# Kernel tuning notes

Hardware: AMD Instinct MI355X
Metric: run time of the kernel (lower is better)

Reference implementation:

```python
import jax, jax.numpy as jnp
import numpy as np

B, C, D, H, W = 8, 256, 128, 64, 64  # batch, in_channels, inter_dim, spatial
BN_EPS = 1e-5


def setup_inputs() -> dict:
    key = jax.random.key(0)
    ks = jax.random.split(key, 6)
    s_c = 1.0 / np.sqrt(C)
    s_d = 1.0 / np.sqrt(D)
    return {
        "x": jax.random.normal(ks[0], (B, C, H, W), dtype=jnp.float32),
        # 1x1 conv kernels, stored as [out_ch, in_ch]
        "theta_w": jax.random.normal(ks[1], (D, C), dtype=jnp.float32) * s_c,
        "phi_w": jax.random.normal(ks[2], (D, C), dtype=jnp.float32) * s_c,
        "g_w": jax.random.normal(ks[3], (D, C), dtype=jnp.float32) * s_c,
        "w_w": jax.random.normal(ks[4], (C, D), dtype=jnp.float32) * s_d,
        "w_b": jnp.zeros((C,), dtype=jnp.float32),
        "bn_gamma": jnp.ones((C,), dtype=jnp.float32),
        "bn_beta": jnp.zeros((C,), dtype=jnp.float32),
    }


def reference(x, theta_w, phi_w, g_w, w_w, w_b, bn_gamma, bn_beta):
    Bs, Cs, Hs, Ws = x.shape
    N = Hs * Ws
    xf = x.reshape(Bs, Cs, N)  # flatten spatial -> [B, C, N]

    # 1x1 convs (bias=False) == per-position channel matmuls
    theta = jnp.einsum('dc,bcn->bnd', theta_w, xf)  # [B, N, D]
    phi = jnp.einsum('dc,bcn->bdn', phi_w, xf)      # [B, D, N]
    g = jnp.einsum('dc,bcn->bnd', g_w, xf)          # [B, N, D]

    # embedded-Gaussian attention: softmax(theta @ phi) @ g
    f = jnp.einsum('bnd,bdm->bnm', theta, phi)      # [B, N, N]
    f_div_C = jax.nn.softmax(f, axis=-1)
    y = jnp.einsum('bnm,bmd->bnd', f_div_C, g)      # [B, N, D]

    # output projection W (1x1 conv with bias)
    w_y = jnp.einsum('cd,bnd->bcn', w_w, y) + w_b[None, :, None]  # [B, C, N]

    # BatchNorm (training mode: batch statistics, biased variance)
    mean = w_y.mean(axis=(0, 2))
    var = jnp.mean(jnp.square(w_y - mean[None, :, None]), axis=(0, 2))
    scale = (bn_gamma * jax.lax.rsqrt(var + BN_EPS))[None, :, None]
    w_y = (w_y - mean[None, :, None]) * scale + bn_beta[None, :, None]

    z = w_y + xf  # residual
    return z.reshape(Bs, Cs, Hs, Ws)
```

## Files before the change

### kernel.cpp

```cpp
#include <hip/hip_runtime.h>

#define BB 8
#define CC 256
#define DD 128
#define NN 4096
#define BN_EPS 1e-5f
#define NSPLIT 4

typedef _Float16 f16;
typedef _Float16 half8 __attribute__((ext_vector_type(8)));
typedef _Float16 half2t __attribute__((ext_vector_type(2)));
typedef float f32x4 __attribute__((ext_vector_type(4)));

__device__ __forceinline__ f32x4 mfma16(half8 a, half8 b, f32x4 c) {
  return __builtin_amdgcn_mfma_f32_16x16x32_f16(a, b, c, 0, 0, 0);
}

__device__ __forceinline__ void gload_lds16(const void* g, void* l) {
  __builtin_amdgcn_global_load_lds((const __attribute__((address_space(1))) void*)g,
                                   (__attribute__((address_space(3))) void*)l, 16, 0, 0);
}

__device__ __forceinline__ half2t pkrtz(float a, float b) {
  auto t = __builtin_amdgcn_cvt_pkrtz(a, b);
  return __builtin_bit_cast(half2t, t);
}

#define EXP2(x) __builtin_amdgcn_exp2f(x)

#define PERM32(i) ((((i) >> 2) & 3) * 8 + (((i) >> 4) & 1) * 4 + ((i) & 3))

__global__ void k_cast_weights(const float* __restrict__ tw, const float* __restrict__ pw,
                               const float* __restrict__ gw, const float* __restrict__ ww,
                               f16* __restrict__ Wcat, f16* __restrict__ Wwh,
                               float* __restrict__ stats) {
  int i = blockIdx.x * 256 + threadIdx.x;
  if (i < 32768) Wcat[i] = (f16)tw[i];
  else if (i < 65536) Wcat[i] = (f16)pw[i - 32768];
  else if (i < 98304) Wcat[i] = (f16)gw[i - 65536];
  else if (i < 131072) Wwh[i - 98304] = (f16)ww[i - 98304];
  if (i < 512) stats[i] = 0.f;
}

__global__ __launch_bounds__(256) void k_gemm1(const float* __restrict__ x, const f16* __restrict__ Wcat,
                                               f16* __restrict__ T, f16* __restrict__ P,
                                               f16* __restrict__ Gdn) {
  __shared__ char xls[32768];
  __shared__ char gls[16384];
  int b = blockIdx.y;
  int n0 = blockIdx.x * 64;
  int tid = threadIdx.x;
  int lane = tid & 63, wave = tid >> 6;
  int lr = lane & 15, lg = lane >> 4;
  int wr = wave >> 1, wc = wave & 1;

  {
    int c = tid;
    const float* src = x + ((size_t)b * CC + c) * NN + n0;
#pragma unroll
    for (int n4 = 0; n4 < 64; n4 += 4) {
      f32x4 v = *(const f32x4*)(src + n4);
#pragma unroll
      for (int k = 0; k < 4; ++k) {
        int n = n4 + k;
        *(f16*)(xls + n * 512 + ((((c >> 3) ^ (n & 7)) * 8 + (c & 7)) * 2)) = (f16)v[k];
      }
    }
  }
  __syncthreads();

  half8 a[2][8];
#pragma unroll
  for (int i = 0; i < 2; ++i) {
    int nloc = wr * 32 + i * 16 + lr;
#pragma unroll
    for (int k0 = 0; k0 < 8; ++k0)
      a[i][k0] = *(const half8*)(xls + nloc * 512 + (((k0 * 4 + lg) ^ (nloc & 7)) << 4));
  }

  size_t base = (size_t)b * NN + n0;
#pragma unroll
  for (int yb = 0; yb < 6; ++yb) {
    int c0 = yb * 64 + wc * 32;
    f32x4 acc[2][2] = {};
#pragma unroll
    for (int k0 = 0; k0 < 8; ++k0) {
      half8 w[2];
      for (int j = 0; j < 2; ++j)
        w[j] = *(const half8*)(Wcat + (size_t)(c0 + j * 16 + lr) * CC + k0 * 32 + lg * 8);
      for (int i = 0; i < 2; ++i)
        for (int j = 0; j < 2; ++j)
          acc[i][j] = mfma16(a[i][k0], w[j], acc[i][j]);
    }
    if (yb < 4) {
      f16* dst = (yb < 2) ? T : P;
      int cl0 = (yb & 1) * 64 + wc * 32;
      for (int i = 0; i < 2; ++i)
        for (int j = 0; j < 2; ++j)
          for (int r = 0; r < 4; ++r) {
            int row = wr * 32 + i * 16 + lg * 4 + r;
            int col = cl0 + j * 16 + lr;
            dst[(base + row) * DD + col] = (f16)acc[i][j][r];
          }
    } else {
      for (int i = 0; i < 2; ++i)
        for (int j = 0; j < 2; ++j)
          for (int r = 0; r < 4; ++r) {
            int n = wr * 32 + i * 16 + lg * 4 + r;
            int d = (yb - 4) * 64 + wc * 32 + j * 16 + lr;
            *(f16*)(gls + n * 256 + ((((d >> 3) ^ (n & 7)) * 8 + (d & 7)) * 2)) = (f16)acc[i][j][r];
          }
    }
  }
  __syncthreads();
  {
    int d = tid >> 1, nh = (tid & 1) * 32;
    f16 tmp[32];
#pragma unroll
    for (int k = 0; k < 32; ++k) {
      int n = nh + k;
      tmp[k] = *(const f16*)(gls + n * 256 + ((((d >> 3) ^ (n & 7)) * 8 + (d & 7)) * 2));
    }
    f16* dst = Gdn + ((size_t)b * DD + d) * NN + n0 + nh;
#pragma unroll
    for (int k = 0; k < 4; ++k)
      *(half8*)(dst + k * 8) = *(const half8*)(tmp + k * 8);
  }
}

__global__ __launch_bounds__(256, 3) void k_flash(const f16* __restrict__ T, const f16* __restrict__ P,
                                                  const f16* __restrict__ Gdn, f16* __restrict__ accs,
                                                  float* __restrict__ ml) {
  __shared__ char smem[32768];
  int bid = blockIdx.x;
  int b = bid & 7;
  int u = bid >> 3;
  int hf = u & 3;
  int qx = u >> 2;
  int t0 = hf * 32;
  const int nt = 32;
  int tid = threadIdx.x;
  int lane = tid & 63, wave = tid >> 6;
  int lr = lane & 15, lg = lane >> 4;
  int q0 = qx * 128 + wave * 32;
  const f16* Tb = T + (size_t)b * NN * DD;
  const f16* Pb = P + ((size_t)b * NN + t0 * 32) * DD;
  const f16* Vb = Gdn + (size_t)b * DD * NN + t0 * 32;
  int srcq = 4 * lg;

  const f16* kbase[2];
  const f16* vbase[2];
  char* kdst[2];
  char* vdst[2];
#pragma unroll
  for (int inst = 0; inst < 2; ++inst) {
    int t = inst * 256 + tid;
    int row = t >> 4, sp = t & 15, sl = sp ^ (row & 7);
    kbase[inst] = Pb + (size_t)PERM32(row) * DD + sl * 8;
    kdst[inst] = smem + (inst * 256 + wave * 64) * 16;
    int dv = t >> 2, gv = t & 3, glv = gv ^ ((dv >> 1) & 3);
    vbase[inst] = Vb + (size_t)dv * NN + glv * 8;
    vdst[inst] = smem + 16384 + (inst * 256 + wave * 64) * 16;
  }

  half8 qf[2][4];
  for (int qt = 0; qt < 2; ++qt)
    for (int ks = 0; ks < 4; ++ks) {
      half8 v = *(const half8*)(Tb + (size_t)(q0 + qt * 16 + lr) * DD + ks * 32 + lg * 8);
      for (int j = 0; j < 8; ++j) v[j] *= (f16)1.44269504f;
      qf[qt][ks] = v;
    }
  half8 ones;
  for (int j = 0; j < 8; ++j) ones[j] = (f16)1.f;

  f32x4 acc[2][8] = {};
  f32x4 lsum[2] = {};
  float m_run[2] = {-1e30f, -1e30f};

#pragma unroll
  for (int inst = 0; inst < 2; ++inst) gload_lds16(kbase[inst], kdst[inst]);
#pragma unroll
  for (int inst = 0; inst < 2; ++inst) gload_lds16(vbase[inst], vdst[inst]);

  for (int kb = 0; kb < nt; ++kb) {
    int keyn = (kb < nt - 1) ? kb * 32 + 32 : 0;
    int cur = (kb & 1) * 8192, nxt = ((kb + 1) & 1) * 8192;
    char* Kc = smem + cur;
    char* Vc = smem + 16384 + cur;

    size_t ko = (size_t)keyn * DD;
#pragma unroll
    for (int inst = 0; inst < 2; ++inst) gload_lds16(kbase[inst] + ko, kdst[inst] + nxt);
    asm volatile("s_waitcnt vmcnt(4)" ::: "memory");
    __builtin_amdgcn_sched_barrier(0);
    __builtin_amdgcn_s_barrier();
    __builtin_amdgcn_sched_barrier(0);

    f32x4 s[2][2];
    __builtin_amdgcn_s_setprio(1);
    for (int kt = 0; kt < 2; ++kt) {
      half8 kf[4];
      for (int ks = 0; ks < 4; ++ks)
        kf[ks] = *(const half8*)(Kc + (kt * 16 + lr) * 256 + (((ks * 4 + lg) ^ (lr & 7)) << 4));
      for (int qt = 0; qt < 2; ++qt) {
        f32x4 t = {};
        for (int ks = 0; ks < 4; ++ks) t = mfma16(kf[ks], qf[qt][ks], t);
        s[qt][kt] = t;
      }
    }
    __builtin_amdgcn_s_setprio(0);

    half8 af[2];
    for (int qt = 0; qt < 2; ++qt) {
      float mx = fmaxf(fmaxf(s[qt][0][0], s[qt][0][1]), fmaxf(s[qt][0][2], s[qt][0][3]));
      mx = fmaxf(mx, fmaxf(fmaxf(s[qt][1][0], s[qt][1][1]), fmaxf(s[qt][1][2], s[qt][1][3])));
      mx = fmaxf(mx, __shfl_xor(mx, 16));
      mx = fmaxf(mx, __shfl_xor(mx, 32));
      bool grow = mx > m_run[qt] + 11.5f;
      if (__ballot(grow)) {
        float mn = fmaxf(m_run[qt], mx);
        float corr = EXP2(m_run[qt] - mn);
        m_run[qt] = mn;
        float c0 = __shfl(corr, srcq + 0), c1 = __shfl(corr, srcq + 1);
        float c2 = __shfl(corr, srcq + 2), c3 = __shfl(corr, srcq + 3);
        lsum[qt][0] *= c0; lsum[qt][1] *= c1; lsum[qt][2] *= c2; lsum[qt][3] *= c3;
        for (int nb = 0; nb < 8; ++nb) {
          acc[qt][nb][0] *= c0; acc[qt][nb][1] *= c1;
          acc[qt][nb][2] *= c2; acc[qt][nb][3] *= c3;
        }
      }
      for (int kt = 0; kt < 2; ++kt)
        for (int r = 0; r < 4; ++r)
          s[qt][kt][r] = EXP2(s[qt][kt][r] - m_run[qt]);
      union { half8 h8; half2t h2[4]; } un;
      un.h2[0] = pkrtz(s[qt][0][0], s[qt][0][1]);
      un.h2[1] = pkrtz(s[qt][0][2], s[qt][0][3]);
      un.h2[2] = pkrtz(s[qt][1][0], s[qt][1][1]);
      un.h2[3] = pkrtz(s[qt][1][2], s[qt][1][3]);
      af[qt] = un.h8;
      lsum[qt] = mfma16(af[qt], ones, lsum[qt]);
    }

#pragma unroll
    for (int inst = 0; inst < 2; ++inst) gload_lds16(vbase[inst] + keyn, vdst[inst] + nxt);
    asm volatile("s_waitcnt vmcnt(4)" ::: "memory");
    __builtin_amdgcn_sched_barrier(0);
    __builtin_amdgcn_s_barrier();
    __builtin_amdgcn_sched_barrier(0);

    __builtin_amdgcn_s_setprio(1);
    for (int nb = 0; nb < 8; ++nb) {
      int d = nb * 16 + lr;
      half8 vf = *(const half8*)(Vc + d * 64 + ((lg ^ ((d >> 1) & 3)) << 4));
      acc[0][nb] = mfma16(af[0], vf, acc[0][nb]);
      acc[1][nb] = mfma16(af[1], vf, acc[1][nb]);
    }
    __builtin_amdgcn_s_setprio(0);
  }
  asm volatile("s_waitcnt vmcnt(0)" ::: "memory");

  size_t gq0 = (size_t)b * NN + q0;
  f16* A = accs + (size_t)hf * ((size_t)BB * NN * DD) + gq0 * DD;
  for (int qt = 0; qt < 2; ++qt)
    for (int nb = 0; nb < 8; ++nb)
      for (int r = 0; r < 4; ++r)
        A[(size_t)(qt * 16 + lg * 4 + r) * DD + nb * 16 + lr] = (f16)acc[qt][nb][r];
  float* mArr = ml + hf * 32768;
  float* lArr = ml + NSPLIT * 32768 + hf * 32768;
  if (lg == 0) {
    mArr[gq0 + lr] = m_run[0];
    mArr[gq0 + 16 + lr] = m_run[1];
  }
  if (lr == 0)
    for (int r = 0; r < 4; ++r) {
      lArr[gq0 + lg * 4 + r] = lsum[0][r];
      lArr[gq0 + 16 + lg * 4 + r] = lsum[1][r];
    }
}

__global__ __launch_bounds__(256) void k_gemm2(const f16* __restrict__ Y, const float* __restrict__ ml,
                                               const f16* __restrict__ Wwh, const float* __restrict__ wb,
                                               f16* __restrict__ wy, float* __restrict__ stats) {
  __shared__ float part[2][8][256];
  const size_t SEG = (size_t)BB * NN * DD;
  int lane = threadIdx.x & 63, wave = threadIdx.x >> 6;
  int lr = lane & 15, lg = lane >> 4;
  int wr = wave >> 1, wc = wave & 1;
  float ps[4][2][2] = {};
  for (int mt = 0; mt < 2; ++mt) {
    int m0 = (blockIdx.x * 2 + mt) * 64 + wr * 32;
    f16 ch[2][NSPLIT];
    for (int i = 0; i < 2; ++i) {
      int row = m0 + i * 16 + lr;
      float m[NSPLIT], l[NSPLIT];
      float mm = -1e30f;
      for (int s = 0; s < NSPLIT; ++s) {
        m[s] = ml[s * 32768 + row];
        l[s] = ml[NSPLIT * 32768 + s * 32768 + row];
        mm = fmaxf(mm, m[s]);
      }
      float den = 0.f, c[NSPLIT];
      for (int s = 0; s < NSPLIT; ++s) {
        c[s] = EXP2(m[s] - mm);
        den += l[s] * c[s];
      }
      float inv = 1.f / den;
      for (int s = 0; s < NSPLIT; ++s) ch[i][s] = (f16)(c[s] * inv);
    }
    half8 a[2][4];
    for (int i = 0; i < 2; ++i)
      for (int k0 = 0; k0 < 4; ++k0) {
        size_t off = (size_t)(m0 + i * 16 + lr) * DD + k0 * 32 + lg * 8;
        half8 acc8 = *(const half8*)(Y + off) * ch[i][0];
        for (int s = 1; s < NSPLIT; ++s)
          acc8 = acc8 + *(const half8*)(Y + s * SEG + off) * ch[i][s];
        a[i][k0] = acc8;
      }
    for (int yb = 0; yb < 4; ++yb) {
      int c0 = yb * 64 + wc * 32;
      f32x4 acc[2][2] = {};
      for (int k0 = 0; k0 < 4; ++k0) {
        half8 w[2];
        for (int j = 0; j < 2; ++j)
          w[j] = *(const half8*)(Wwh + (size_t)(c0 + j * 16 + lr) * DD + k0 * 32 + lg * 8);
        for (int i = 0; i < 2; ++i)
          for (int j = 0; j < 2; ++j)
            acc[i][j] = mfma16(a[i][k0], w[j], acc[i][j]);
      }
      for (int i = 0; i < 2; ++i)
        for (int j = 0; j < 2; ++j) {
          float bias = wb[c0 + j * 16 + lr];
          for (int r = 0; r < 4; ++r) {
            int row = m0 + i * 16 + lg * 4 + r;
            int col = c0 + j * 16 + lr;
            float v = acc[i][j][r] + bias;
            wy[(size_t)row * CC + col] = (f16)v;
            ps[yb][j][0] += v;
            ps[yb][j][1] += v * v;
          }
        }
    }
  }
  for (int yb = 0; yb < 4; ++yb)
    for (int j = 0; j < 2; ++j) {
      int col = yb * 64 + wc * 32 + j * 16 + lr;
      part[0][wr * 4 + lg][col] = ps[yb][j][0];
      part[1][wr * 4 + lg][col] = ps[yb][j][1];
    }
  __syncthreads();
  {
    int col = threadIdx.x;
    for (int metric = 0; metric < 2; ++metric) {
      float s = 0.f;
      for (int wtr = 0; wtr < 8; ++wtr) s += part[metric][wtr][col];
      atomicAdd(&stats[metric * CC + col], s);
    }
  }
}

__global__ void k_bn_apply(const f16* __restrict__ wy, const float* __restrict__ x,
                           const float* __restrict__ stats, const float* __restrict__ gamma,
                           const float* __restrict__ beta, float* __restrict__ out) {
  __shared__ f16 tile[32][33];
  int b = blockIdx.z, c0 = blockIdx.y * 32, n0 = blockIdx.x * 32;
  int tx = threadIdx.x, ty = threadIdx.y;
  for (int j = 0; j < 4; ++j) {
    int nn = ty + j * 8;
    tile[nn][tx] = wy[((size_t)b * NN + n0 + nn) * CC + c0 + tx];
  }
  __syncthreads();
  const float inv_cnt = 1.f / (float)(BB * NN);
  for (int j = 0; j < 4; ++j) {
    int cc = ty + j * 8;
    int c = c0 + cc;
    float mean = stats[c] * inv_cnt;
    float var = stats[CC + c] * inv_cnt - mean * mean;
    float scale = gamma[c] * rsqrtf(var + BN_EPS);
    size_t oi = ((size_t)b * CC + c) * NN + n0 + tx;
    out[oi] = ((float)tile[tx][cc] - mean) * scale + beta[c] + x[oi];
  }
}

extern "C" void kernel_launch(void* const* d_in, const int* in_sizes, int n_in,
                              void* d_out, int out_size, void* d_ws, size_t ws_size,
                              hipStream_t stream) {
  const float* x = (const float*)d_in[0];
  const float* tw = (const float*)d_in[1];
  const float* pw = (const float*)d_in[2];
  const float* gw = (const float*)d_in[3];
  const float* ww = (const float*)d_in[4];
  const float* wb = (const float*)d_in[5];
  const float* gamma = (const float*)d_in[6];
  const float* beta = (const float*)d_in[7];
  float* out = (float*)d_out;
  char* ws = (char*)d_ws;

  f16* Wcat = (f16*)(ws + 0);
  f16* Wwh = (f16*)(ws + 196608);
  float* stats = (float*)(ws + 262144);
  float* ml = (float*)(ws + 524288);
  const size_t BASE = 1 << 21;
  f16* T = (f16*)(ws + BASE);
  f16* P = (f16*)(ws + BASE + 8388608);
  f16* Gdn = (f16*)(ws + BASE + 16777216);
  f16* accs = (f16*)(ws + BASE + 25165824);
  f16* wy = (f16*)(ws + BASE);

  k_cast_weights<<<512, 256, 0, stream>>>(tw, pw, gw, ww, Wcat, Wwh, stats);
  k_gemm1<<<dim3(NN / 64, BB), 256, 0, stream>>>(x, Wcat, T, P, Gdn);
  k_flash<<<1024, 256, 0, stream>>>(T, P, Gdn, accs, ml);
  k_gemm2<<<256, 256, 0, stream>>>(accs, ml, Wwh, wb, wy, stats);
  k_bn_apply<<<dim3(NN / 32, CC / 32, BB), dim3(32, 8), 0, stream>>>(wy, x, stats, gamma, beta, out);
}
```

Before: 167.3 us.

## Split flash KV range three ways and vectorize BN-apply transpose

Changes the flash-attention key/value split from four to three chunks (43/43/42 tiles of 32), reducing the grid from 1024 to 768 blocks so it better matches CU count and occupancy and cuts partial-result merge work. The BN-apply kernel is rewritten to process a 64-position by 256-channel tile per block with half8 loads and float4 loads/stores, replacing scalar 32x32 tiles. The uneven split and the gemm2 merge must agree on NSPLIT. The LDS transpose writes may cause bank conflicts.

New measurement: 161.3 us. 1.04x faster.

```diff
diff --git a/kernel.cpp b/kernel.cpp
--- a/kernel.cpp
+++ b/kernel.cpp
@@ -5,10 +5,11 @@
 #define DD 128
 #define NN 4096
 #define BN_EPS 1e-5f
-#define NSPLIT 4
+#define NSPLIT 3
 
 typedef _Float16 f16;
 typedef _Float16 half8 __attribute__((ext_vector_type(8)));
+typedef _Float16 half4 __attribute__((ext_vector_type(4)));
 typedef _Float16 half2t __attribute__((ext_vector_type(2)));
 typedef float f32x4 __attribute__((ext_vector_type(4)));
 
@@ -135,10 +136,10 @@
   int bid = blockIdx.x;
   int b = bid & 7;
   int u = bid >> 3;
-  int hf = u & 3;
-  int qx = u >> 2;
-  int t0 = hf * 32;
-  const int nt = 32;
+  int hf = u % 3;
+  int qx = u / 3;
+  int t0 = (hf == 2) ? 86 : hf * 43;
+  int nt = (hf == 2) ? 42 : 43;
   int tid = threadIdx.x;
   int lane = tid & 63, wave = tid >> 6;
   int lr = lane & 15, lg = lane >> 4;
@@ -358,26 +359,47 @@
   }
 }
 
-__global__ void k_bn_apply(const f16* __restrict__ wy, const float* __restrict__ x,
-                           const float* __restrict__ stats, const float* __restrict__ gamma,
-                           const float* __restrict__ beta, float* __restrict__ out) {
-  __shared__ f16 tile[32][33];
-  int b = blockIdx.z, c0 = blockIdx.y * 32, n0 = blockIdx.x * 32;
-  int tx = threadIdx.x, ty = threadIdx.y;
-  for (int j = 0; j < 4; ++j) {
-    int nn = ty + j * 8;
-    tile[nn][tx] = wy[((size_t)b * NN + n0 + nn) * CC + c0 + tx];
+__global__ __launch_bounds__(256) void k_bn_apply(const f16* __restrict__ wy, const float* __restrict__ x,
+                                                  const float* __restrict__ stats, const float* __restrict__ gamma,
+                                                  const float* __restrict__ beta, float* __restrict__ out) {
+  __shared__ f16 tile[256][68];
+  int b = blockIdx.y, n0 = blockIdx.x * 64;
+  int t = threadIdx.x;
+  size_t base = (size_t)b * NN;
+#pragma unroll
+  for (int it = 0; it < 4; ++it) {
+    int n = it * 16 + (t >> 4);
+    int cg = t & 15;
+    const f16* src = wy + (base + n0 + n) * CC;
+    half8 v0 = *(const half8*)(src + cg * 8);
+    half8 v1 = *(const half8*)(src + 128 + cg * 8);
+#pragma unroll
+    for (int k = 0; k < 8; ++k) {
+      tile[cg * 8 + k][n] = v0[k];
+      tile[128 + cg * 8 + k][n] = v1[k];
+    }
   }
   __syncthreads();
   const float inv_cnt = 1.f / (float)(BB * NN);
-  for (int j = 0; j < 4; ++j) {
-    int cc = ty + j * 8;
-    int c = c0 + cc;
+#pragma unroll
+  for (int cc = 0; cc < 4; ++cc) {
+    int c = cc * 64 + (t >> 2);
+    int nq = (t & 3) * 16;
     float mean = stats[c] * inv_cnt;
     float var = stats[CC + c] * inv_cnt - mean * mean;
     float scale = gamma[c] * rsqrtf(var + BN_EPS);
-    size_t oi = ((size_t)b * CC + c) * NN + n0 + tx;
-    out[oi] = ((float)tile[tx][cc] - mean) * scale + beta[c] + x[oi];
+    float bet = beta[c];
+    size_t oi = ((size_t)b * CC + c) * NN + n0 + nq;
+#pragma unroll
+    for (int g = 0; g < 4; ++g) {
+      half4 wv = *(const half4*)&tile[c][nq + g * 4];
+      f32x4 xa = *(const f32x4*)(x + oi + g * 4);
+      f32x4 o;
+#pragma unroll
+      for (int k = 0; k < 4; ++k)
+        o[k] = ((float)wv[k] - mean) * scale + bet + xa[k];
+      *(f32x4*)(out + oi + g * 4) = o;
+    }
   }
 }
 
@@ -408,7 +430,7 @@
 
   k_cast_weights<<<512, 256, 0, stream>>>(tw, pw, gw, ww, Wcat, Wwh, stats);
   k_gemm1<<<dim3(NN / 64, BB), 256, 0, stream>>>(x, Wcat, T, P, Gdn);
-  k_flash<<<1024, 256, 0, stream>>>(T, P, Gdn, accs, ml);
+  k_flash<<<768, 256, 0, stream>>>(T, P, Gdn, accs, ml);
   k_gemm2<<<256, 256, 0, stream>>>(accs, ml, Wwh, wb, wy, stats);
-  k_bn_apply<<<dim3(NN / 32, CC / 32, BB), dim3(32, 8), 0, stream>>>(wy, x, stats, gamma, beta, out);
-}
+  k_bn_apply<<<dim3(NN / 64, BB), 256, 0, stream>>>(wy, x, stats, gamma, beta, out);
+}
```
